# Performance work log

Measured on AMD Instinct MI355X. Metric: run time of the kernel, lower is better.

## Reference

```python
import jax, jax.numpy as jnp
import numpy as np

# dims
N, E, Z, C, NB = 8192, 131072, 10, 128, 8
R_MAX, P_CUT, AVG_NEIGH = 5.0, 5, 16.0
SH_DIM, N_L, N_LAYERS, MLP_H = 16, 4, 2, 16
# which l each of the 16 sh components belongs to
L_OF_M = jnp.array([0, 1, 1, 1, 2, 2, 2, 2, 2, 3, 3, 3, 3, 3, 3, 3])


def spherical_harmonics(u):
    """Real spherical harmonics up to l=3, e3nn 'component' normalization. u: [E,3] unit vectors."""
    x, y, z = u[:, 0], u[:, 1], u[:, 2]
    x2, y2, z2 = x * x, y * y, z * z
    s3, s5, s15 = np.sqrt(3.0), np.sqrt(5.0), np.sqrt(15.0)
    a33, a32, a31, a30 = 0.25 * np.sqrt(70.0), np.sqrt(105.0), 0.25 * np.sqrt(42.0), 0.5 * np.sqrt(7.0)
    Y = [jnp.ones_like(x),
         s3 * x, s3 * y, s3 * z,
         s15 * x * y, s15 * y * z, 0.5 * s5 * (3 * z2 - 1.0), s15 * x * z, 0.5 * s15 * (x2 - y2),
         a33 * y * (3 * x2 - y2), a32 * x * y * z, a31 * y * (5 * z2 - 1.0),
         a30 * z * (5 * z2 - 3.0), a31 * x * (5 * z2 - 1.0), 0.5 * a32 * z * (x2 - y2),
         a33 * x * (x2 - 3 * y2)]
    return jnp.stack(Y, axis=-1)  # [E,16]


def radial_embedding(r):
    """Bessel radial basis with smooth polynomial cutoff (p=5). r: [E] edge lengths."""
    x = r / R_MAX
    p = float(P_CUT)
    cut = (1.0 - 0.5 * (p + 1.0) * (p + 2.0) * x ** P_CUT
           + p * (p + 2.0) * x ** (P_CUT + 1) - 0.5 * p * (p + 1.0) * x ** (P_CUT + 2))
    cut = jnp.where(x < 1.0, cut, 0.0)
    n = jnp.arange(1, NB + 1, dtype=r.dtype)
    bessel = np.sqrt(2.0 / R_MAX) * jnp.sin(n[None, :] * jnp.pi * x[:, None]) / r[:, None]
    return bessel * cut[:, None]  # [E,8]


def _forward(positions, node_attrs, shifts, W_embed, W_up, R_w1, R_w2, R_w3,
             W_out, w_sc, w_prod, W_plin, w_ro0, ro_w1, ro_w2, edge_index):
    sender, receiver = edge_index[0], edge_index[1]
    vec = positions[receiver] - positions[sender] + shifts          # [E,3]
    lengths = jnp.linalg.norm(vec, axis=-1) + 1e-9                  # [E]
    sh = spherical_harmonics(vec / lengths[:, None])                # [E,16]
    edge_feats = radial_embedding(lengths)                          # [E,8]

    # node embedding: scalars into l=0 slot of [N,C,16]
    scalars = node_attrs @ W_embed                                  # [N,C]
    feats = jnp.zeros((N, C, SH_DIM), scalars.dtype).at[:, :, 0].set(scalars)

    outputs = []
    for L in range(N_LAYERS):
        # linear up (channel mixing, per irrep component)
        h = jnp.einsum('ncm,cd->ndm', feats, W_up[L])               # [N,C,16]
        # radial MLP -> per-edge, per-channel, per-l tensor-product weights
        r = jax.nn.silu(edge_feats @ R_w1[L])
        r = jax.nn.silu(r @ R_w2[L])
        w = (r @ R_w3[L]).reshape(E, C, N_L)                        # [E,C,4]
        w_m = jnp.take(w, L_OF_M, axis=2)                           # [E,C,16]
        # channel-wise tensor product: scalar node feat x SH, scatter to receiver
        msg = h[sender, :, 0][:, :, None] * w_m * sh[:, None, :]    # [E,C,16]
        agg = jax.ops.segment_sum(msg, receiver, num_segments=N) / AVG_NEIGH
        m = jnp.einsum('ncm,cd->ndm', agg, W_out[L])                # [N,C,16]
        # element-dependent skip connection
        sc = h * (node_attrs @ w_sc[L])[:, :, None]
        # product basis (correlation 3): element-weighted powers of scalar part
        s = m[:, :, 0]                                              # [N,C]
        coeff = jnp.einsum('nz,zck->nck', node_attrs, w_prod[L])    # [N,C,3]
        powers = jnp.stack([jnp.ones_like(s), s, s * s], axis=-1)   # [N,C,3]
        scale = jnp.sum(coeff * powers, axis=-1)                    # [N,C]
        feats = jnp.einsum('ncm,cd->ndm', m * scale[:, :, None], W_plin[L]) + sc
        if L == 0:
            outputs.append(feats[:, :, 0] @ w_ro0)                  # linear readout [N]
        else:
            outputs.append(jax.nn.silu(feats[:, :, 0] @ ro_w1) @ ro_w2)  # nonlinear readout [N]
    return outputs[0] + outputs[1]


def setup_inputs() -> dict:
    key = jax.random.key(0)
    ks = jax.random.split(key, 16)
    positions = jax.random.normal(ks[0], (N, 3), jnp.float32) * 1.5
    elems = jax.random.randint(ks[1], (N,), 0, Z)
    node_attrs = jax.nn.one_hot(elems, Z, dtype=jnp.float32)
    edge_index = jax.random.randint(ks[2], (2, E), 0, N)
    shifts = jnp.zeros((E, 3), jnp.float32)
    g = lambda k, sh, fan: jax.random.normal(k, sh, jnp.float32) / np.sqrt(fan)
    return {
        'positions': positions, 'node_attrs': node_attrs, 'shifts': shifts,
        'W_embed': g(ks[3], (Z, C), Z),
        'W_up': g(ks[4], (N_LAYERS, C, C), C),
        'R_w1': g(ks[5], (N_LAYERS, NB, 64), NB),
        'R_w2': g(ks[6], (N_LAYERS, 64, 64), 64),
        'R_w3': g(ks[7], (N_LAYERS, 64, C * N_L), 64),
        'W_out': g(ks[8], (N_LAYERS, C, C), C),
        'w_sc': g(ks[9], (N_LAYERS, Z, C), 1),
        'w_prod': g(ks[10], (N_LAYERS, Z, C, 3), 1) * 0.1,
        'W_plin': g(ks[11], (N_LAYERS, C, C), C),
        'w_ro0': g(ks[12], (C,), C),
        'ro_w1': g(ks[13], (C, MLP_H), C),
        'ro_w2': g(ks[14], (MLP_H,), MLP_H),
        'edge_index': edge_index,
    }


def reference(positions, node_attrs, shifts, W_embed, W_up, R_w1, R_w2, R_w3,
              W_out, w_sc, w_prod, W_plin, w_ro0, ro_w1, ro_w2, edge_index):
    return _forward(positions, node_attrs, shifts, W_embed, W_up, R_w1, R_w2, R_w3,
                    W_out, w_sc, w_prod, W_plin, w_ro0, ro_w1, ro_w2, edge_index)
```

## Files before the change

kernel.cpp:

```cpp
#include <hip/hip_runtime.h>
#include <math.h>

constexpr int kN = 8192;
constexpr int kE = 131072;
constexpr int kHalfN = 4096;
constexpr int kWbTiles = 544;
constexpr int kWbRows  = kWbTiles * 128;

typedef short bf16x8 __attribute__((ext_vector_type(8)));
typedef float f32x4 __attribute__((ext_vector_type(4)));
typedef unsigned short ushort_t;
typedef unsigned int uint_t;

__device__ __forceinline__ float silu_f(float x) { return x / (1.f + __expf(-x)); }

__device__ __forceinline__ ushort_t f2b(float f) {
  uint_t x = __float_as_uint(f);
  uint_t r = (x + 0x7fffu + ((x >> 16) & 1u)) >> 16;
  return (ushort_t)r;
}
__device__ __forceinline__ float b2f(ushort_t u) {
  return __uint_as_float(((uint_t)u) << 16);
}

__global__ __launch_bounds__(256) void zero_ints_kernel(int* __restrict__ a, int* __restrict__ b) {
  int i = blockIdx.x * 256 + threadIdx.x;
  if (i < kN) { a[i] = 0; b[i] = 0; }
}

__global__ __launch_bounds__(256) void elem_kernel(const float* __restrict__ attrs, int* __restrict__ elem) {
  int n = blockIdx.x * 256 + threadIdx.x;
  if (n >= kN) return;
  const float* a = attrs + (size_t)n * 10;
  int best = 0; float bv = a[0];
  #pragma unroll
  for (int z = 1; z < 10; ++z) { float v = a[z]; if (v > bv) { bv = v; best = z; } }
  elem[n] = best;
}

__global__ __launch_bounds__(256) void init_feats_kernel(const float* __restrict__ W_embed,
                                                         const int* __restrict__ elem,
                                                         ushort_t* __restrict__ F) {
  int i = blockIdx.x * 256 + threadIdx.x;
  int n = i >> 7, c = i & 127;
  F[(size_t)n * 2048 + c] = f2b(W_embed[(size_t)elem[n] * 128 + c]);
}

__global__ __launch_bounds__(256) void geom_kernel(const float* __restrict__ pos,
                                                   const float* __restrict__ shifts,
                                                   const int* __restrict__ ei,
                                                   float* __restrict__ sh,
                                                   float* __restrict__ rb) {
  int e = blockIdx.x * 256 + threadIdx.x;
  if (e >= kE) return;
  int s = ei[e], r = ei[kE + e];
  float vx = pos[r*3+0] - pos[s*3+0] + shifts[(size_t)e*3+0];
  float vy = pos[r*3+1] - pos[s*3+1] + shifts[(size_t)e*3+1];
  float vz = pos[r*3+2] - pos[s*3+2] + shifts[(size_t)e*3+2];
  float len = sqrtf(vx*vx + vy*vy + vz*vz) + 1e-9f;
  float inv = 1.f / len;
  float x = vx*inv, y = vy*inv, z = vz*inv;
  float x2 = x*x, y2 = y*y, z2 = z*z;
  const float s3  = 1.7320508075688772f;
  const float s5  = 2.2360679774997896f;
  const float s15 = 3.8729833462074170f;
  const float a33 = 2.0916500663351889f;
  const float a32 = 10.246950765959598f;
  const float a31 = 1.6201851746019651f;
  const float a30 = 1.3228756555322954f;
  float4* shp = (float4*)(sh + (size_t)e * 16);
  shp[0] = make_float4(1.f, s3*x, s3*y, s3*z);
  shp[1] = make_float4(s15*x*y, s15*y*z, 0.5f*s5*(3.f*z2 - 1.f), s15*x*z);
  shp[2] = make_float4(0.5f*s15*(x2 - y2), a33*y*(3.f*x2 - y2), a32*x*y*z, a31*y*(5.f*z2 - 1.f));
  shp[3] = make_float4(a30*z*(5.f*z2 - 3.f), a31*x*(5.f*z2 - 1.f), 0.5f*a32*z*(x2 - y2), a33*x*(x2 - 3.f*y2));
  float xr = len * 0.2f;
  float cut = 0.f;
  if (xr < 1.f) {
    float x5 = xr*xr*xr*xr*xr;
    cut = 1.f - 21.f*x5 + 35.f*x5*xr - 15.f*x5*xr*xr;
  }
  float pref = 0.63245553203367587f * cut * inv;
  const float PI = 3.14159265358979323846f;
  float b[8];
  #pragma unroll
  for (int k = 0; k < 8; ++k) b[k] = pref * sinf((float)(k+1) * PI * xr);
  float4* rbp = (float4*)(rb + (size_t)e * 8);
  rbp[0] = make_float4(b[0], b[1], b[2], b[3]);
  rbp[1] = make_float4(b[4], b[5], b[6], b[7]);
}

__global__ __launch_bounds__(256) void count_kernel(const int* __restrict__ ei, int* __restrict__ counts) {
  int e = blockIdx.x * 256 + threadIdx.x;
  if (e < kE) atomicAdd(&counts[ei[kE + e]], 1);
}

__global__ __launch_bounds__(1024) void scan_kernel(const int* __restrict__ counts, int* __restrict__ offs) {
  __shared__ int tmp[1024];
  int t = threadIdx.x;
  int loc[8]; int s = 0;
  #pragma unroll
  for (int i = 0; i < 8; ++i) { loc[i] = s; s += counts[t*8 + i]; }
  tmp[t] = s;
  __syncthreads();
  for (int d = 1; d < 1024; d <<= 1) {
    int v = (t >= d) ? tmp[t - d] : 0;
    __syncthreads();
    tmp[t] += v;
    __syncthreads();
  }
  int pre = (t == 0) ? 0 : tmp[t - 1];
  #pragma unroll
  for (int i = 0; i < 8; ++i) offs[t*8 + i] = pre + loc[i];
  if (t == 1023) offs[kN] = tmp[1023];
}

__global__ __launch_bounds__(256) void fill_kernel(const int* __restrict__ ei, const int* __restrict__ offs,
                                                   int* __restrict__ cursor, int* __restrict__ eids) {
  int e = blockIdx.x * 256 + threadIdx.x;
  if (e >= kE) return;
  int r = ei[kE + e];
  int pos = atomicAdd(&cursor[r], 1);
  eids[offs[r] + pos] = e;
}

constexpr int kEB = 32;
__global__ __launch_bounds__(256) void radial_kernel(const float* __restrict__ rb,
                                                     const float* __restrict__ W1,
                                                     const float* __restrict__ W2,
                                                     ushort_t* __restrict__ r2) {
  __shared__ float W1s[8*64];
  __shared__ float W2s[64*64];
  __shared__ float r1s[2][4][64];
  int tid = threadIdx.x;
  for (int i = tid; i < 512; i += 256) W1s[i] = W1[i];
  for (int i = tid; i < 4096; i += 256) W2s[i] = W2[i];
  int g = tid >> 6, j = tid & 63;
  __syncthreads();
  #pragma unroll
  for (int cch = 0; cch < kEB/4; ++cch) {
    int e = blockIdx.x * kEB + cch * 4 + g;
    const float* rbe = rb + (size_t)e * 8;
    float v = 0.f;
    #pragma unroll
    for (int i = 0; i < 8; ++i) v = fmaf(rbe[i], W1s[i*64 + j], v);
    r1s[cch & 1][g][j] = silu_f(v);
    __syncthreads();
    float u = 0.f;
    #pragma unroll
    for (int i = 0; i < 64; ++i) u = fmaf(r1s[cch & 1][g][i], W2s[i*64 + j], u);
    r2[(size_t)e * 64 + j] = f2b(silu_f(u));
  }
}

__global__ __launch_bounds__(256) void transpose_w_kernel(const float* __restrict__ W, ushort_t* __restrict__ WT) {
  int i = blockIdx.x * 256 + threadIdx.x;
  int d = i >> 7, c = i & 127;
  WT[i] = f2b(W[c*128 + d]);
}

__global__ __launch_bounds__(256) void transpose_r3_kernel(const float* __restrict__ R3, ushort_t* __restrict__ R3T) {
  int i = blockIdx.x * 256 + threadIdx.x;
  int t = i >> 6, j = i & 63;
  R3T[i] = f2b(R3[j*512 + t]);
}

template<bool SCALED, bool EPI, bool L0>
__global__ __launch_bounds__(256) void mgemm_kernel(
    const ushort_t* __restrict__ A, size_t aStride,
    const ushort_t* __restrict__ BT,
    ushort_t* __restrict__ O, size_t oStride,
    const float* __restrict__ scaleBuf,
    const ushort_t* __restrict__ Hbuf,
    const float* __restrict__ wscL,
    const int* __restrict__ elem)
{
  __shared__ ushort_t As[128][136];
  __shared__ ushort_t Bs[128][136];
  const int tid = threadIdx.x;
  const size_t rowbase = (size_t)blockIdx.x * 128;

  for (int idx = tid * 8; idx < 128 * 128; idx += 256 * 8) {
    int r = idx >> 7, k = idx & 127;
    *(int4*)&Bs[r][k] = *(const int4*)&BT[(size_t)r * 128 + k];
  }
  for (int idx = tid * 8; idx < 128 * 128; idx += 256 * 8) {
    int r = idx >> 7, k = idx & 127;
    size_t grow = rowbase + r;
    const ushort_t* ap = A + grow * aStride + k;
    if (SCALED) {
      const float* sp = scaleBuf + (grow >> 4) * 128 + k;
      uint_t u[4];
      #pragma unroll
      for (int q = 0; q < 4; ++q) {
        ushort_t lo = f2b(b2f(ap[2*q])   * sp[2*q]);
        ushort_t hi = f2b(b2f(ap[2*q+1]) * sp[2*q+1]);
        u[q] = (uint_t)lo | ((uint_t)hi << 16);
      }
      *(int4*)&As[r][k] = make_int4((int)u[0], (int)u[1], (int)u[2], (int)u[3]);
    } else {
      *(int4*)&As[r][k] = *(const int4*)ap;
    }
  }
  __syncthreads();

  const int lane = tid & 63, wv = tid >> 6;
  const int wr = (wv >> 1) * 64, wc = (wv & 1) * 64;
  const int fr = lane & 15;
  const int kg = (lane >> 4) * 8;
  f32x4 acc[4][4] = {};
  #pragma unroll
  for (int ks = 0; ks < 4; ++ks) {
    const int k0 = ks * 32 + kg;
    bf16x8 af[4], bfr[4];
    #pragma unroll
    for (int i = 0; i < 4; ++i) af[i]  = *(const bf16x8*)&As[wr + i*16 + fr][k0];
    #pragma unroll
    for (int j = 0; j < 4; ++j) bfr[j] = *(const bf16x8*)&Bs[wc + j*16 + fr][k0];
    #pragma unroll
    for (int i = 0; i < 4; ++i)
      #pragma unroll
      for (int j = 0; j < 4; ++j)
        acc[i][j] = __builtin_amdgcn_mfma_f32_16x16x32_bf16(af[i], bfr[j], acc[i][j], 0, 0, 0);
  }

  const int dcol = lane & 15, drow4 = (lane >> 4) * 4;
  #pragma unroll
  for (int i = 0; i < 4; ++i) {
    #pragma unroll
    for (int j = 0; j < 4; ++j) {
      int col = wc + j*16 + dcol;
      #pragma unroll
      for (int r = 0; r < 4; ++r) {
        int row = wr + i*16 + drow4 + r;
        size_t grow = rowbase + row;
        float v = acc[i][j][r];
        if (EPI) {
          if (!L0 || ((grow & 15) == 0)) {
            int ee = elem[grow >> 4];
            v += b2f(Hbuf[grow * 128 + col]) * wscL[(size_t)ee * 128 + col];
          }
        }
        O[grow * oStride + col] = f2b(v);
      }
    }
  }
}

__global__ __launch_bounds__(256) void wgemm_kernel(
    const ushort_t* __restrict__ r2, const int* __restrict__ eids,
    const int* __restrict__ offs, int nb0,
    const ushort_t* __restrict__ R3T, ushort_t* __restrict__ wb)
{
  __shared__ ushort_t As[128][72];
  __shared__ ushort_t Bs[128][72];
  const int tid = threadIdx.x;
  const int rowbase = blockIdx.x * 128;
  const int colbase = blockIdx.y * 128;
  const int halfStart = offs[nb0];
  const int halfEnd   = offs[nb0 + kHalfN];

  for (int idx = tid * 8; idx < 128 * 64; idx += 256 * 8) {
    int r = idx >> 6, k = idx & 63;
    *(int4*)&Bs[r][k] = *(const int4*)&R3T[(size_t)(colbase + r) * 64 + k];
  }
  for (int idx = tid * 8; idx < 128 * 64; idx += 256 * 8) {
    int r = idx >> 6, k = idx & 63;
    int ii = halfStart + rowbase + r;
    int iic = ii < halfEnd ? ii : (halfEnd - 1);
    if (iic < 0) iic = 0;
    int e = eids[iic];
    *(int4*)&As[r][k] = *(const int4*)&r2[(size_t)e * 64 + k];
  }
  __syncthreads();

  const int lane = tid & 63, wv = tid >> 6;
  const int wr = (wv >> 1) * 64, wc = (wv & 1) * 64;
  const int fr = lane & 15;
  const int kg = (lane >> 4) * 8;
  f32x4 acc[4][4] = {};
  #pragma unroll
  for (int ks = 0; ks < 2; ++ks) {
    const int k0 = ks * 32 + kg;
    bf16x8 af[4], bfr[4];
    #pragma unroll
    for (int i = 0; i < 4; ++i) af[i]  = *(const bf16x8*)&As[wr + i*16 + fr][k0];
    #pragma unroll
    for (int j = 0; j < 4; ++j) bfr[j] = *(const bf16x8*)&Bs[wc + j*16 + fr][k0];
    #pragma unroll
    for (int i = 0; i < 4; ++i)
      #pragma unroll
      for (int j = 0; j < 4; ++j)
        acc[i][j] = __builtin_amdgcn_mfma_f32_16x16x32_bf16(af[i], bfr[j], acc[i][j], 0, 0, 0);
  }

  const int dcol = lane & 15, drow4 = (lane >> 4) * 4;
  #pragma unroll
  for (int i = 0; i < 4; ++i) {
    #pragma unroll
    for (int j = 0; j < 4; ++j) {
      int col = colbase + wc + j*16 + dcol;
      #pragma unroll
      for (int r = 0; r < 4; ++r) {
        int row = rowbase + wr + i*16 + drow4 + r;
        wb[(size_t)row * 512 + col] = f2b(acc[i][j][r]);
      }
    }
  }
}

constexpr int CH = 16;
__global__ __launch_bounds__(512) void gather_kernel(
    const int* __restrict__ offs, const int* __restrict__ eids,
    const int* __restrict__ ei, int nb0,
    const ushort_t* __restrict__ wb,
    const float* __restrict__ sh,
    const ushort_t* __restrict__ H,
    ushort_t* __restrict__ AGG)
{
  __shared__ ushort_t ws[CH][512];
  __shared__ ushort_t h0s[CH][128];
  __shared__ float shs[CH][16];
  int n = nb0 + blockIdx.x;
  int t = threadIdx.x;
  int l = t >> 7;
  int c = t & 127;
  const int wstart = offs[nb0];
  float a0=0,a1=0,a2=0,a3=0,a4=0,a5=0,a6=0;
  const int e0 = offs[n], e1 = offs[n+1];
  for (int base = e0; base < e1; base += CH) {
    const int cnt = min(CH, e1 - base);
    #pragma unroll
    for (int rep = 0; rep < 2; ++rep) {
      int idx = rep * 512 + t;
      int j = idx >> 6, seg = idx & 63;
      if (j < cnt)
        *(int4*)&ws[j][seg * 8] = *(const int4*)&wb[(size_t)(base - wstart + j) * 512 + seg * 8];
    }
    if (t < 256) {
      int j = t >> 4, seg = t & 15;
      if (j < cnt) {
        int e = eids[base + j];
        *(int4*)&h0s[j][seg * 8] = *(const int4*)&H[(size_t)ei[e] * 2048 + seg * 8];
      }
    } else if (t < 320) {
      int tt = t - 256, j = tt >> 2, seg = tt & 3;
      if (j < cnt)
        *(float4*)&shs[j][seg * 4] = *(const float4*)&sh[(size_t)eids[base + j] * 16 + seg * 4];
    }
    __syncthreads();
    for (int j = 0; j < cnt; ++j) {
      float wv = b2f(ws[j][(c << 2) | l]);
      float wh = wv * b2f(h0s[j][c]);
      if (l == 0) {
        a0 = fmaf(wh, shs[j][0], a0);
      } else if (l == 1) {
        float4 s4 = *(const float4*)&shs[j][0];
        a0 = fmaf(wh, s4.y, a0); a1 = fmaf(wh, s4.z, a1); a2 = fmaf(wh, s4.w, a2);
      } else if (l == 2) {
        float4 s4 = *(const float4*)&shs[j][4];
        float s8 = shs[j][8];
        a0 = fmaf(wh, s4.x, a0); a1 = fmaf(wh, s4.y, a1); a2 = fmaf(wh, s4.z, a2);
        a3 = fmaf(wh, s4.w, a3); a4 = fmaf(wh, s8, a4);
      } else {
        float4 sA = *(const float4*)&shs[j][8];
        float4 sB = *(const float4*)&shs[j][12];
        a0 = fmaf(wh, sA.y, a0); a1 = fmaf(wh, sA.z, a1); a2 = fmaf(wh, sA.w, a2);
        a3 = fmaf(wh, sB.x, a3); a4 = fmaf(wh, sB.y, a4); a5 = fmaf(wh, sB.z, a5);
        a6 = fmaf(wh, sB.w, a6);
      }
    }
    __syncthreads();
  }
  const float inv16 = 0.0625f;
  size_t baseo = (size_t)n * 2048 + c;
  if (l == 0) {
    AGG[baseo] = f2b(a0 * inv16);
  } else if (l == 1) {
    AGG[baseo + 1*128] = f2b(a0*inv16); AGG[baseo + 2*128] = f2b(a1*inv16); AGG[baseo + 3*128] = f2b(a2*inv16);
  } else if (l == 2) {
    AGG[baseo + 4*128] = f2b(a0*inv16); AGG[baseo + 5*128] = f2b(a1*inv16); AGG[baseo + 6*128] = f2b(a2*inv16);
    AGG[baseo + 7*128] = f2b(a3*inv16); AGG[baseo + 8*128] = f2b(a4*inv16);
  } else {
    AGG[baseo + 9*128]  = f2b(a0*inv16); AGG[baseo + 10*128] = f2b(a1*inv16); AGG[baseo + 11*128] = f2b(a2*inv16);
    AGG[baseo + 12*128] = f2b(a3*inv16); AGG[baseo + 13*128] = f2b(a4*inv16); AGG[baseo + 14*128] = f2b(a5*inv16);
    AGG[baseo + 15*128] = f2b(a6*inv16);
  }
}

__global__ __launch_bounds__(256) void scale_kernel(const ushort_t* __restrict__ M,
                                                    const int* __restrict__ elem,
                                                    const float* __restrict__ wprodL,
                                                    float* __restrict__ scale) {
  int i = blockIdx.x * 256 + threadIdx.x;
  int n = i >> 7, c = i & 127;
  float s = b2f(M[(size_t)n * 2048 + c]);
  const float* co = wprodL + ((size_t)elem[n] * 128 + c) * 3;
  scale[i] = co[0] + s * (co[1] + s * co[2]);
}

__global__ __launch_bounds__(64) void readout_kernel(const ushort_t* __restrict__ F,
                                                     const float* __restrict__ ro0,
                                                     const float* __restrict__ ro1,
                                                     const float* __restrict__ ro2,
                                                     float* __restrict__ out, int layer) {
  int n = blockIdx.x; int t = threadIdx.x;
  const ushort_t* fr = F + (size_t)n * 2048;
  float f0 = b2f(fr[t]), f1 = b2f(fr[t + 64]);
  if (layer == 0) {
    float v = f0 * ro0[t] + f1 * ro0[t + 64];
    #pragma unroll
    for (int m = 32; m > 0; m >>= 1) v += __shfl_xor(v, m, 64);
    if (t == 0) out[n] = v;
  } else {
    float acc = 0.f;
    for (int h = 0; h < 16; ++h) {
      float p = f0 * ro1[t*16 + h] + f1 * ro1[(t + 64)*16 + h];
      #pragma unroll
      for (int m = 32; m > 0; m >>= 1) p += __shfl_xor(p, m, 64);
      acc = fmaf(silu_f(p), ro2[h], acc);
    }
    if (t == 0) out[n] += acc;
  }
}

extern "C" void kernel_launch(void* const* d_in, const int* in_sizes, int n_in,
                              void* d_out, int out_size, void* d_ws, size_t ws_size,
                              hipStream_t stream) {
  (void)in_sizes; (void)n_in; (void)out_size;
  const float* positions = (const float*)d_in[0];
  const float* node_attrs= (const float*)d_in[1];
  const float* shifts    = (const float*)d_in[2];
  const float* W_embed   = (const float*)d_in[3];
  const float* W_up      = (const float*)d_in[4];
  const float* R_w1      = (const float*)d_in[5];
  const float* R_w2      = (const float*)d_in[6];
  const float* R_w3      = (const float*)d_in[7];
  const float* W_out     = (const float*)d_in[8];
  const float* w_sc      = (const float*)d_in[9];
  const float* w_prod    = (const float*)d_in[10];
  const float* W_plin    = (const float*)d_in[11];
  const float* w_ro0     = (const float*)d_in[12];
  const float* ro_w1     = (const float*)d_in[13];
  const float* ro_w2     = (const float*)d_in[14];
  const int*   ei        = (const int*)d_in[15];
  float* out = (float*)d_out;

  char* ws_ptr = (char*)d_ws;
  size_t off = 0;
  auto alloc = [&](size_t nbytes) -> void* {
    void* p = ws_ptr + off;
    off += (nbytes + 255) & ~(size_t)255;
    return p;
  };
  const size_t PB = (size_t)kN * 16 * 128 * sizeof(ushort_t);
  ushort_t* P0   = (ushort_t*)alloc(PB);
  ushort_t* P1   = (ushort_t*)alloc(PB);
  ushort_t* P2   = (ushort_t*)alloc(PB);
  float* shb     = (float*)alloc((size_t)kE * 16 * 4);
  float* rbb     = (float*)alloc((size_t)kE * 8 * 4);
  ushort_t* r2b  = (ushort_t*)alloc((size_t)kE * 64 * 2);
  float* scaleb  = (float*)alloc((size_t)kN * 128 * 4);
  ushort_t* wb   = (ushort_t*)alloc((size_t)kWbRows * 512 * 2);
  ushort_t* R3T0 = (ushort_t*)alloc(512 * 64 * 2);
  ushort_t* R3T1 = (ushort_t*)alloc(512 * 64 * 2);
  ushort_t* WTu0 = (ushort_t*)alloc(128 * 128 * 2);
  ushort_t* WTu1 = (ushort_t*)alloc(128 * 128 * 2);
  ushort_t* WTo0 = (ushort_t*)alloc(128 * 128 * 2);
  ushort_t* WTo1 = (ushort_t*)alloc(128 * 128 * 2);
  ushort_t* WTp0 = (ushort_t*)alloc(128 * 128 * 2);
  ushort_t* WTp1 = (ushort_t*)alloc(128 * 128 * 2);
  int* elemb  = (int*)alloc(kN * 4);
  int* counts = (int*)alloc(kN * 4);
  int* cursor = (int*)alloc(kN * 4);
  int* offsb  = (int*)alloc((kN + 1) * 4);
  int* eidsb  = (int*)alloc((size_t)kE * 4);
  if (off > ws_size) return;

  zero_ints_kernel<<<kN/256, 256, 0, stream>>>(counts, cursor);
  elem_kernel<<<kN/256, 256, 0, stream>>>(node_attrs, elemb);
  init_feats_kernel<<<(kN*128)/256, 256, 0, stream>>>(W_embed, elemb, P0);
  geom_kernel<<<kE/256, 256, 0, stream>>>(positions, shifts, ei, shb, rbb);
  count_kernel<<<kE/256, 256, 0, stream>>>(ei, counts);
  scan_kernel<<<1, 1024, 0, stream>>>(counts, offsb);
  fill_kernel<<<kE/256, 256, 0, stream>>>(ei, offsb, cursor, eidsb);
  transpose_w_kernel<<<64, 256, 0, stream>>>(W_up, WTu0);
  transpose_w_kernel<<<64, 256, 0, stream>>>(W_up + 16384, WTu1);
  transpose_w_kernel<<<64, 256, 0, stream>>>(W_out, WTo0);
  transpose_w_kernel<<<64, 256, 0, stream>>>(W_out + 16384, WTo1);
  transpose_w_kernel<<<64, 256, 0, stream>>>(W_plin, WTp0);
  transpose_w_kernel<<<64, 256, 0, stream>>>(W_plin + 16384, WTp1);
  transpose_r3_kernel<<<128, 256, 0, stream>>>(R_w3, R3T0);
  transpose_r3_kernel<<<128, 256, 0, stream>>>(R_w3 + 32768, R3T1);

  radial_kernel<<<kE/kEB, 256, 0, stream>>>(rbb, R_w1, R_w2, r2b);
  mgemm_kernel<false,false,false><<<kN/128, 256, 0, stream>>>(
      P0, 2048, WTu0, P1, 2048, nullptr, nullptr, nullptr, nullptr);
  wgemm_kernel<<<dim3(kWbTiles,4), 256, 0, stream>>>(r2b, eidsb, offsb, 0, R3T0, wb);
  gather_kernel<<<kHalfN, 512, 0, stream>>>(offsb, eidsb, ei, 0, wb, shb, P1, P2);
  wgemm_kernel<<<dim3(kWbTiles,4), 256, 0, stream>>>(r2b, eidsb, offsb, kHalfN, R3T0, wb);
  gather_kernel<<<kHalfN, 512, 0, stream>>>(offsb, eidsb, ei, kHalfN, wb, shb, P1, P2);
  mgemm_kernel<false,false,false><<<(kN*16)/128, 256, 0, stream>>>(
      P2, 128, WTo0, P0, 128, nullptr, nullptr, nullptr, nullptr);
  scale_kernel<<<(kN*128)/256, 256, 0, stream>>>(P0, elemb, w_prod, scaleb);
  mgemm_kernel<true,true,true><<<(kN*16)/128, 256, 0, stream>>>(
      P0, 128, WTp0, P2, 128, scaleb, P1, w_sc, elemb);
  readout_kernel<<<kN, 64, 0, stream>>>(P2, w_ro0, ro_w1, ro_w2, out, 0);

  radial_kernel<<<kE/kEB, 256, 0, stream>>>(rbb, R_w1 + 512, R_w2 + 4096, r2b);
  mgemm_kernel<false,false,false><<<(kN*16)/128, 256, 0, stream>>>(
      P2, 128, WTu1, P1, 128, nullptr, nullptr, nullptr, nullptr);
  wgemm_kernel<<<dim3(kWbTiles,4), 256, 0, stream>>>(r2b, eidsb, offsb, 0, R3T1, wb);
  gather_kernel<<<kHalfN, 512, 0, stream>>>(offsb, eidsb, ei, 0, wb, shb, P1, P0);
  wgemm_kernel<<<dim3(kWbTiles,4), 256, 0, stream>>>(r2b, eidsb, offsb, kHalfN, R3T1, wb);
  gather_kernel<<<kHalfN, 512, 0, stream>>>(offsb, eidsb, ei, kHalfN, wb, shb, P1, P0);
  mgemm_kernel<false,false,false><<<(kN*16)/128, 256, 0, stream>>>(
      P0, 128, WTo1, P2, 128, nullptr, nullptr, nullptr, nullptr);
  scale_kernel<<<(kN*128)/256, 256, 0, stream>>>(P2, elemb, w_prod + 3840, scaleb);
  mgemm_kernel<true,true,false><<<(kN*16)/128, 256, 0, stream>>>(
      P2, 128, WTp1, P0, 128, scaleb, P1, w_sc + 1280, elemb);
  readout_kernel<<<kN, 64, 0, stream>>>(P0, w_ro0, ro_w1, ro_w2, out, 1);
}
```

Measured before the change: 548.0 us.

## Use MFMA for radial MLP second layer and sine recurrence for Bessel basis

The radial MLP kernel now handles 128 edges per block. It stages the first-layer output and a transposed bf16 copy of W2 in shared memory, then runs the 64x64 second layer with bf16 MFMA instructions instead of scalar FMAs, and writes results out with vectorized stores. The geometry kernel replaces eight sinf calls with one __sincosf followed by the Chebyshev recurrence for sin(k*theta). The change cuts ALU work and per-block weight reloads, but the hidden activation is now rounded to bf16 before the second layer, and the recurrence with fast sincos adds a small numerical error.

```diff
diff --git a/kernel.cpp b/kernel.cpp
--- a/kernel.cpp
+++ b/kernel.cpp
@@ -81,9 +81,19 @@
   }
   float pref = 0.63245553203367587f * cut * inv;
   const float PI = 3.14159265358979323846f;
+  float theta = PI * xr;
+  float sn, cs;
+  __sincosf(theta, &sn, &cs);
+  float twoc = 2.f * cs;
   float b[8];
-  #pragma unroll
-  for (int k = 0; k < 8; ++k) b[k] = pref * sinf((float)(k+1) * PI * xr);
+  float s_prev = 0.f, s_cur = sn;
+  b[0] = pref * s_cur;
+  #pragma unroll
+  for (int k = 1; k < 8; ++k) {
+    float s_next = twoc * s_cur - s_prev;
+    s_prev = s_cur; s_cur = s_next;
+    b[k] = pref * s_cur;
+  }
   float4* rbp = (float4*)(rb + (size_t)e * 8);
   rbp[0] = make_float4(b[0], b[1], b[2], b[3]);
   rbp[1] = make_float4(b[4], b[5], b[6], b[7]);
@@ -123,32 +133,73 @@
   eids[offs[r] + pos] = e;
 }
 
-constexpr int kEB = 32;
 __global__ __launch_bounds__(256) void radial_kernel(const float* __restrict__ rb,
                                                      const float* __restrict__ W1,
                                                      const float* __restrict__ W2,
                                                      ushort_t* __restrict__ r2) {
+  __shared__ float rbs[128][8];
   __shared__ float W1s[8*64];
-  __shared__ float W2s[64*64];
-  __shared__ float r1s[2][4][64];
-  int tid = threadIdx.x;
+  __shared__ ushort_t B2s[64][72];
+  __shared__ ushort_t r1s[128][72];
+  const int tid = threadIdx.x;
+  const size_t ebase = (size_t)blockIdx.x * 128;
+  {
+    int r = tid >> 1, q = tid & 1;
+    *(float4*)&rbs[r][q*4] = *(const float4*)&rb[(ebase + r)*8 + q*4];
+  }
   for (int i = tid; i < 512; i += 256) W1s[i] = W1[i];
-  for (int i = tid; i < 4096; i += 256) W2s[i] = W2[i];
-  int g = tid >> 6, j = tid & 63;
-  __syncthreads();
-  #pragma unroll
-  for (int cch = 0; cch < kEB/4; ++cch) {
-    int e = blockIdx.x * kEB + cch * 4 + g;
-    const float* rbe = rb + (size_t)e * 8;
-    float v = 0.f;
-    #pragma unroll
-    for (int i = 0; i < 8; ++i) v = fmaf(rbe[i], W1s[i*64 + j], v);
-    r1s[cch & 1][g][j] = silu_f(v);
-    __syncthreads();
-    float u = 0.f;
-    #pragma unroll
-    for (int i = 0; i < 64; ++i) u = fmaf(r1s[cch & 1][g][i], W2s[i*64 + j], u);
-    r2[(size_t)e * 64 + j] = f2b(silu_f(u));
+  for (int i = tid; i < 4096; i += 256) {
+    int k = i >> 6, col = i & 63;
+    B2s[col][k] = f2b(W2[i]);
+  }
+  __syncthreads();
+  {
+    int col = tid & 63;
+    int r0 = (tid >> 6) * 32;
+    #pragma unroll 4
+    for (int rr = 0; rr < 32; ++rr) {
+      int row = r0 + rr;
+      float v = 0.f;
+      #pragma unroll
+      for (int i = 0; i < 8; ++i) v = fmaf(rbs[row][i], W1s[i*64 + col], v);
+      r1s[row][col] = f2b(silu_f(v));
+    }
+  }
+  __syncthreads();
+  const int lane = tid & 63, wv = tid >> 6;
+  const int wr = wv * 32;
+  const int fr = lane & 15, kg = (lane >> 4) * 8;
+  f32x4 acc[2][4] = {};
+  #pragma unroll
+  for (int ks = 0; ks < 2; ++ks) {
+    const int k0 = ks*32 + kg;
+    bf16x8 af[2], bfr[4];
+    #pragma unroll
+    for (int i = 0; i < 2; ++i) af[i] = *(const bf16x8*)&r1s[wr + i*16 + fr][k0];
+    #pragma unroll
+    for (int j = 0; j < 4; ++j) bfr[j] = *(const bf16x8*)&B2s[j*16 + fr][k0];
+    #pragma unroll
+    for (int i = 0; i < 2; ++i)
+      #pragma unroll
+      for (int j = 0; j < 4; ++j)
+        acc[i][j] = __builtin_amdgcn_mfma_f32_16x16x32_bf16(af[i], bfr[j], acc[i][j], 0, 0, 0);
+  }
+  __syncthreads();
+  const int dcol = lane & 15, drow4 = (lane >> 4) * 4;
+  #pragma unroll
+  for (int i = 0; i < 2; ++i)
+    #pragma unroll
+    for (int j = 0; j < 4; ++j)
+      #pragma unroll
+      for (int r = 0; r < 4; ++r) {
+        int row = wr + i*16 + drow4 + r;
+        int col = j*16 + dcol;
+        r1s[row][col] = f2b(silu_f(acc[i][j][r]));
+      }
+  __syncthreads();
+  for (int idx = tid * 8; idx < 128*64; idx += 256*8) {
+    int r = idx >> 6, k = idx & 63;
+    *(int4*)&r2[(ebase + r)*64 + k] = *(const int4*)&r1s[r][k];
   }
 }
 
@@ -492,7 +543,7 @@
   transpose_r3_kernel<<<128, 256, 0, stream>>>(R_w3, R3T0);
   transpose_r3_kernel<<<128, 256, 0, stream>>>(R_w3 + 32768, R3T1);
 
-  radial_kernel<<<kE/kEB, 256, 0, stream>>>(rbb, R_w1, R_w2, r2b);
+  radial_kernel<<<kE/128, 256, 0, stream>>>(rbb, R_w1, R_w2, r2b);
   mgemm_kernel<false,false,false><<<kN/128, 256, 0, stream>>>(
       P0, 2048, WTu0, P1, 2048, nullptr, nullptr, nullptr, nullptr);
   wgemm_kernel<<<dim3(kWbTiles,4), 256, 0, stream>>>(r2b, eidsb, offsb, 0, R3T0, wb);
@@ -506,7 +557,7 @@
       P0, 128, WTp0, P2, 128, scaleb, P1, w_sc, elemb);
   readout_kernel<<<kN, 64, 0, stream>>>(P2, w_ro0, ro_w1, ro_w2, out, 0);
 
-  radial_kernel<<<kE/kEB, 256, 0, stream>>>(rbb, R_w1 + 512, R_w2 + 4096, r2b);
+  radial_kernel<<<kE/128, 256, 0, stream>>>(rbb, R_w1 + 512, R_w2 + 4096, r2b);
   mgemm_kernel<false,false,false><<<(kN*16)/128, 256, 0, stream>>>(
       P2, 128, WTu1, P1, 128, nullptr, nullptr, nullptr, nullptr);
   wgemm_kernel<<<dim3(kWbTiles,4), 256, 0, stream>>>(r2b, eidsb, offsb, 0, R3T1, wb);
```

New measurement: 471.1 us. -14.0%, faster.
